# Kernel optimization log

Hardware: AMD Instinct MI355X
Metric: run time of the kernel (lower is better)

Reference implementation:

```python
import jax, jax.numpy as jnp
import numpy as np

N_EMBED = 1024
N_HEAD = 16
EPS = 1.1920929e-07  # torch.finfo(float32).eps, nn.RMSNorm default eps=None


def rmsnorm(x, w):
    var = jnp.mean(x * x, axis=-1, keepdims=True)
    return x * jax.lax.rsqrt(var + EPS) * w


def setup_inputs() -> dict:
    key = jax.random.key(0)
    ks = jax.random.split(key, 12)
    d = N_EMBED
    s = lambda fan_in: 1.0 / np.sqrt(fan_in)
    inp = {
        "x": jax.random.normal(ks[0], (2, 2048, d), jnp.float32),
        "w_attn": jax.random.uniform(ks[1], (d, 3 * d), jnp.float32, -s(d), s(d)),
        "b_attn": jax.random.uniform(ks[2], (3 * d,), jnp.float32, -s(d), s(d)),
        "w_proj": jax.random.uniform(ks[3], (d, d), jnp.float32, -s(d), s(d)),
        "b_proj": jax.random.uniform(ks[4], (d,), jnp.float32, -s(d), s(d)),
        "w_fc1": jax.random.uniform(ks[5], (d, 4 * d), jnp.float32, -s(d), s(d)),
        "b_fc1": jax.random.uniform(ks[6], (4 * d,), jnp.float32, -s(d), s(d)),
        "w_fc2": jax.random.uniform(ks[7], (4 * d, d), jnp.float32, -s(4 * d), s(4 * d)),
        "b_fc2": jax.random.uniform(ks[8], (d,), jnp.float32, -s(4 * d), s(4 * d)),
        "g_norm1": jnp.ones((d,), jnp.float32),
        "g_norm2": jnp.ones((d,), jnp.float32),
    }
    return inp


def reference(x, w_attn, b_attn, w_proj, b_proj, w_fc1, b_fc1, w_fc2, b_fc2, g_norm1, g_norm2):
    B, T, d = x.shape
    H = N_HEAD
    hd = d // H

    # --- attention branch ---
    h = rmsnorm(x, g_norm1)
    qkv = h @ w_attn + b_attn  # [B,T,3d]
    q, k, v = jnp.split(qkv, 3, axis=-1)
    q = q.reshape(B, T, H, hd).transpose(0, 2, 1, 3)  # [B,H,T,hd]
    k = k.reshape(B, T, H, hd).transpose(0, 2, 1, 3)
    v = v.reshape(B, T, H, hd).transpose(0, 2, 1, 3)
    qk = jnp.einsum('bhqd,bhkd->bhqk', q, k)  # NOTE: no logit scaling (as in source)
    mask = jnp.tril(jnp.ones((T, T), bool))
    qk = jnp.where(mask, qk, -jnp.inf)
    # source scales softmax OUTPUT by n_embed**-0.5 (faithful quirk)
    attn = jax.nn.softmax(qk, axis=-1) * (d ** -0.5)
    o = jnp.einsum('bhqk,bhkd->bhqd', attn, v)
    o = o.transpose(0, 2, 1, 3).reshape(B, T, d)
    x = x + (o @ w_proj + b_proj)

    # --- MLP branch ---
    h = rmsnorm(x, g_norm2)
    h = jax.nn.gelu(h @ w_fc1 + b_fc1, approximate=False)
    x = x + (h @ w_fc2 + b_fc2)
    return x
```

## Files before the change

### kernel.cpp

```cpp
#include <hip/hip_runtime.h>
#include <hip/hip_bf16.h>


typedef __hip_bfloat16 bf16;
typedef __attribute__((ext_vector_type(8))) short short8;
typedef __attribute__((ext_vector_type(4))) float floatx4;

__device__ __forceinline__ float bits2f(unsigned short u) {
  union { unsigned int i; float f; } c; c.i = ((unsigned int)u) << 16; return c.f;
}
__device__ __forceinline__ unsigned short f2bits(float f) {
  bf16 b = __float2bfloat16(f);
  union { bf16 b; unsigned short u; } c; c.b = b; return c.u;
}

__device__ __forceinline__ void gld_lds16(const unsigned short* g, unsigned short* l) {
  __builtin_amdgcn_global_load_lds(
      (const __attribute__((address_space(1))) void*)g,
      (__attribute__((address_space(3))) void*)l, 16, 0, 0);
}

__global__ __launch_bounds__(256) void rmsnorm_r18(const float* __restrict__ x,
                                                   const float* __restrict__ g,
                                                   unsigned short* __restrict__ out)
{
  const int row = blockIdx.x, tid = threadIdx.x;
  const size_t rb = (size_t)row * 1024;
  float4 xv = *(const float4*)(x + rb + tid * 4);
  float v[4] = {xv.x, xv.y, xv.z, xv.w};
  float s = v[0]*v[0] + v[1]*v[1] + v[2]*v[2] + v[3]*v[3];
  #pragma unroll
  for (int off = 32; off > 0; off >>= 1) s += __shfl_down(s, off, 64);
  __shared__ float part[4];
  if ((tid & 63) == 0) part[tid >> 6] = s;
  __syncthreads();
  const float tot = part[0] + part[1] + part[2] + part[3];
  const float sc = rsqrtf(tot * (1.0f / 1024.0f) + 1.1920929e-07f);
  float4 gv = *(const float4*)(g + tid * 4);
  ushort4 o4 = { f2bits(v[0] * sc * gv.x), f2bits(v[1] * sc * gv.y),
                 f2bits(v[2] * sc * gv.z), f2bits(v[3] * sc * gv.w) };
  *(ushort4*)(out + rb + tid * 4) = o4;
}

__global__ __launch_bounds__(256) void wprep_r18(const float* __restrict__ in,
                                                 unsigned short* __restrict__ out,
                                                 int K, int N)
{
  __shared__ unsigned short tile[32][33];
  const int tid = threadIdx.x;
  const int k0 = blockIdx.y * 32, n0 = blockIdx.x * 32;
  const int tr = tid >> 3, tc4 = (tid & 7) * 4;
  float4 v = *(const float4*)(in + (size_t)(k0 + tr) * N + n0 + tc4);
  tile[tr][tc4 + 0] = f2bits(v.x);
  tile[tr][tc4 + 1] = f2bits(v.y);
  tile[tr][tc4 + 2] = f2bits(v.z);
  tile[tr][tc4 + 3] = f2bits(v.w);
  __syncthreads();
  ushort4 o = { tile[tc4 + 0][tr], tile[tc4 + 1][tr],
                tile[tc4 + 2][tr], tile[tc4 + 3][tr] };
  *(ushort4*)(out + (size_t)(n0 + tr) * K + k0 + tc4) = o;
}

template<int EPI>
__global__ __launch_bounds__(256) void gemm128_r18(
    const unsigned short* __restrict__ A,
    const unsigned short* __restrict__ BT,
    const float* __restrict__ bias,
    const float* __restrict__ resid,
    void* __restrict__ Cout,
    int M, int N, int K, int Klen)
{
  __shared__ __align__(16) unsigned short As[2][128 * 32];
  __shared__ __align__(16) unsigned short Bs[2][128 * 32];
  const int tid = threadIdx.x;
  const int lane = tid & 63;
  const int wv = tid >> 6;
  const int m0 = blockIdx.y * 128, n0 = blockIdx.x * 128;
  const int wm = (wv >> 1) * 64, wn = (wv & 1) * 64;
  const int kbase = blockIdx.z * Klen;

  const int s0 = tid, s1 = tid + 256;
  const int r0 = s0 >> 2, kq0 = (s0 & 3) ^ ((r0 >> 1) & 3);
  const int r1 = s1 >> 2, kq1 = (s1 & 3) ^ ((r1 >> 1) & 3);
  const unsigned short* Ab = A  + (size_t)m0 * K;
  const unsigned short* Bb = BT + (size_t)n0 * K;
  const size_t ga0 = (size_t)r0 * K + kq0 * 8 + kbase;
  const size_t ga1 = (size_t)r1 * K + kq1 * 8 + kbase;

  floatx4 acc[4][4];
  #pragma unroll
  for (int i = 0; i < 4; ++i)
    #pragma unroll
    for (int j = 0; j < 4; ++j)
      acc[i][j] = (floatx4){0.f, 0.f, 0.f, 0.f};

  int aoff[4], boff[4];
  #pragma unroll
  for (int i = 0; i < 4; ++i) {
    int ra = wm + i * 16 + (lane & 15);
    aoff[i] = (ra * 4 + ((lane >> 4) ^ ((ra >> 1) & 3))) * 8;
    int rb = wn + i * 16 + (lane & 15);
    boff[i] = (rb * 4 + ((lane >> 4) ^ ((rb >> 1) & 3))) * 8;
  }

  gld_lds16(Ab + ga0, As[0] + s0 * 8);
  gld_lds16(Ab + ga1, As[0] + s1 * 8);
  gld_lds16(Bb + ga0, Bs[0] + s0 * 8);
  gld_lds16(Bb + ga1, Bs[0] + s1 * 8);
  __syncthreads();

  const int nsteps = Klen >> 5;
  for (int t = 0; t < nsteps; ++t) {
    const int cur = t & 1;
    if (t + 1 < nsteps) {
      const size_t ko = (size_t)(t + 1) * 32;
      gld_lds16(Ab + ga0 + ko, As[cur ^ 1] + s0 * 8);
      gld_lds16(Ab + ga1 + ko, As[cur ^ 1] + s1 * 8);
      gld_lds16(Bb + ga0 + ko, Bs[cur ^ 1] + s0 * 8);
      gld_lds16(Bb + ga1 + ko, Bs[cur ^ 1] + s1 * 8);
    }

    short8 af[4], bfr[4];
    #pragma unroll
    for (int i = 0; i < 4; ++i) {
      af[i]  = *(const short8*)(As[cur] + aoff[i]);
      bfr[i] = *(const short8*)(Bs[cur] + boff[i]);
    }
    #pragma unroll
    for (int i = 0; i < 4; ++i)
      #pragma unroll
      for (int j = 0; j < 4; ++j)
        acc[i][j] = __builtin_amdgcn_mfma_f32_16x16x32_bf16(af[i], bfr[j], acc[i][j], 0, 0, 0);

    __syncthreads();
  }

  float* Cp32 = (float*)Cout;
  if constexpr (EPI == 4) Cp32 += (size_t)blockIdx.z * ((size_t)M * N);

  #pragma unroll
  for (int i = 0; i < 4; ++i) {
    #pragma unroll
    for (int j = 0; j < 4; ++j) {
      const int rbase = m0 + wm + i * 16 + (lane >> 4) * 4;
      const int c = n0 + wn + j * 16 + (lane & 15);
      float bia = 0.0f;
      if constexpr (EPI != 4) bia = bias[c];
      #pragma unroll
      for (int r = 0; r < 4; ++r) {
        float v = acc[i][j][r] + bia;
        const size_t idx = (size_t)(rbase + r) * N + c;
        if constexpr (EPI == 0) {
          ((unsigned short*)Cout)[idx] = f2bits(v);
        } else if constexpr (EPI == 1) {
          ((float*)Cout)[idx] = v + resid[idx];
        } else if constexpr (EPI == 2) {
          v = 0.5f * v * (1.0f + erff(v * 0.70710678118654752f));
          ((unsigned short*)Cout)[idx] = f2bits(v);
        } else if constexpr (EPI == 3) {
          ((float*)Cout)[idx] = v + resid[idx];
        } else {
          Cp32[idx] = v;
        }
      }
    }
  }
}

template<int EPI>
__global__ __launch_bounds__(512) void gemm256_r18(
    const unsigned short* __restrict__ A,
    const unsigned short* __restrict__ BT,
    const float* __restrict__ bias,
    void* __restrict__ Cout,
    int M, int N, int K)
{
  __shared__ __align__(16) unsigned short As[4][256 * 32];
  __shared__ __align__(16) unsigned short Bs[4][256 * 32];
  const int tid = threadIdx.x;
  const int lane = tid & 63, wv = tid >> 6;
  const int quad = lane >> 4, l15 = lane & 15;
  const int m0 = blockIdx.y * 256, n0 = blockIdx.x * 256;
  const int wm = (wv >> 2) * 128, wn = (wv & 3) * 64;

  const int s0 = tid, s1 = tid + 512;
  const int r0 = s0 >> 2, kq0 = (s0 & 3) ^ ((r0 >> 1) & 3);
  const int r1 = s1 >> 2, kq1 = (s1 & 3) ^ ((r1 >> 1) & 3);
  const unsigned short* Ab = A  + (size_t)m0 * K;
  const unsigned short* Bb = BT + (size_t)n0 * K;
  const size_t ga0 = (size_t)r0 * K + kq0 * 8;
  const size_t ga1 = (size_t)r1 * K + kq1 * 8;

  floatx4 acc[8][4];
  #pragma unroll
  for (int i = 0; i < 8; ++i)
    #pragma unroll
    for (int j = 0; j < 4; ++j)
      acc[i][j] = (floatx4){0.f, 0.f, 0.f, 0.f};

  int aoff[8], boff[4];
  #pragma unroll
  for (int i = 0; i < 8; ++i) {
    int ra = wm + i * 16 + l15;
    aoff[i] = (ra * 4 + (quad ^ ((ra >> 1) & 3))) * 8;
  }
  #pragma unroll
  for (int j = 0; j < 4; ++j) {
    int rb = wn + j * 16 + l15;
    boff[j] = (rb * 4 + (quad ^ ((rb >> 1) & 3))) * 8;
  }

  #define STG_R18(t) { const size_t ko = (size_t)(t) * 32; const int bb = (t) & 3; \
    gld_lds16(Ab + ga0 + ko, As[bb] + s0 * 8); \
    gld_lds16(Ab + ga1 + ko, As[bb] + s1 * 8); \
    gld_lds16(Bb + ga0 + ko, Bs[bb] + s0 * 8); \
    gld_lds16(Bb + ga1 + ko, Bs[bb] + s1 * 8); }

  STG_R18(0);
  STG_R18(1);

  const int nsteps = K >> 5;
  for (int t = 0; t < nsteps; ++t) {
    const int cur = t & 3;
    if (t + 2 < nsteps) {
      STG_R18(t + 2);
      asm volatile("s_waitcnt vmcnt(8)" ::: "memory");
    } else if (t + 1 < nsteps) {
      asm volatile("s_waitcnt vmcnt(4)" ::: "memory");
    } else {
      asm volatile("s_waitcnt vmcnt(0)" ::: "memory");
    }
    __builtin_amdgcn_s_barrier();
    asm volatile("" ::: "memory");

    short8 bfr[4];
    #pragma unroll
    for (int j = 0; j < 4; ++j)
      bfr[j] = *(const short8*)(Bs[cur] + boff[j]);
    #pragma unroll
    for (int ih = 0; ih < 2; ++ih) {
      short8 af[4];
      #pragma unroll
      for (int k = 0; k < 4; ++k)
        af[k] = *(const short8*)(As[cur] + aoff[ih * 4 + k]);
      #pragma unroll
      for (int k = 0; k < 4; ++k)
        #pragma unroll
        for (int j = 0; j < 4; ++j)
          acc[ih * 4 + k][j] = __builtin_amdgcn_mfma_f32_16x16x32_bf16(af[k], bfr[j], acc[ih * 4 + k][j], 0, 0, 0);
    }
  }
  #undef STG_R18

  #pragma unroll
  for (int i = 0; i < 8; ++i) {
    #pragma unroll
    for (int j = 0; j < 4; ++j) {
      const int rbase = m0 + wm + i * 16 + quad * 4;
      const int c = n0 + wn + j * 16 + l15;
      const float bia = bias[c];
      #pragma unroll
      for (int r = 0; r < 4; ++r) {
        float v = acc[i][j][r] + bia;
        const size_t idx = (size_t)(rbase + r) * N + c;
        if constexpr (EPI == 2) {
          v = 0.5f * v * (1.0f + erff(v * 0.70710678118654752f));
        }
        ((unsigned short*)Cout)[idx] = f2bits(v);
      }
    }
  }
}

__global__ __launch_bounds__(256) void red2_r18(const float* __restrict__ P,
                                                const float* __restrict__ resid,
                                                const float* __restrict__ bias,
                                                float* __restrict__ out)
{
  const size_t i = ((size_t)blockIdx.x * 256 + threadIdx.x) * 4;
  const int col = (int)(i & 1023);
  float4 p0 = *(const float4*)(P + i);
  float4 p1 = *(const float4*)(P + ((size_t)4096 * 1024) + i);
  float4 xr = *(const float4*)(resid + i);
  float4 b  = *(const float4*)(bias + col);
  float4 o  = { p0.x + p1.x + xr.x + b.x, p0.y + p1.y + xr.y + b.y,
                p0.z + p1.z + xr.z + b.z, p0.w + p1.w + xr.w + b.w };
  *(float4*)(out + i) = o;
}

__global__ __launch_bounds__(512) void attn_r18(const unsigned short* __restrict__ qkv,
                                                unsigned short* __restrict__ o)
{
  __shared__ __align__(16) unsigned short Qs[128 * 64];
  __shared__ __align__(16) unsigned short Ks[2][128 * 64];
  __shared__ __align__(16) unsigned short VT[2][64 * 136];
  __shared__ __align__(16) unsigned short Ps[128 * 136];
  __shared__ __align__(16) float stat_s[128];

  const int tid = threadIdx.x, lane = tid & 63, wv = tid >> 6;
  const int quad = lane >> 4, l15 = lane & 15;
  const int qt0 = blockIdx.x, bh = blockIdx.y;
  const int b = bh >> 4, h = bh & 15;
  const size_t base = (size_t)b * 2048 * 3072;
  const int qcol = h * 64, kcol = 1024 + h * 64, vcol = 2048 + h * 64;

  const int sr = tid >> 3, scp = tid & 7, sc = scp ^ (sr & 7);
  const unsigned short* kgp = qkv + base + (size_t)sr * 3072 + kcol + sc * 8;
  const int vp = tid & 63, vdc = tid >> 6;
  const unsigned short* vgp = qkv + base + (size_t)(2 * vp) * 3072 + vcol + vdc * 8;

  for (int pass = 0; pass < 2; ++pass) {
    const int qt = pass ? qt0 : 15 - qt0;
    const int q0 = qt * 128;
    const int nkt = qt + 1;

    __syncthreads();

    #pragma unroll
    for (int p = 0; p < 2; ++p) {
      int s = tid + 512 * p;
      int r = s >> 3, cp = s & 7, c = cp ^ (r & 7);
      gld_lds16(qkv + base + (size_t)(q0 + r) * 3072 + qcol + c * 8, Qs + s * 8);
    }
    gld_lds16(kgp, Ks[0] + tid * 8);
    gld_lds16(kgp + (size_t)64 * 3072, Ks[0] + (size_t)(tid + 512) * 8);
    {
      uint4 u0 = *(const uint4*)vgp;
      uint4 u1 = *(const uint4*)(vgp + 3072);
      unsigned short* dst = VT[0] + (size_t)(vdc * 8) * 136 + 2 * vp;
      *(unsigned int*)(dst + 0 * 136) = (u0.x & 0xffffu) | (u1.x << 16);
      *(unsigned int*)(dst + 1 * 136) = (u0.x >> 16)     | (u1.x & 0xffff0000u);
      *(unsigned int*)(dst + 2 * 136) = (u0.y & 0xffffu) | (u1.y << 16);
      *(unsigned int*)(dst + 3 * 136) = (u0.y >> 16)     | (u1.y & 0xffff0000u);
      *(unsigned int*)(dst + 4 * 136) = (u0.z & 0xffffu) | (u1.z << 16);
      *(unsigned int*)(dst + 5 * 136) = (u0.z >> 16)     | (u1.z & 0xffff0000u);
      *(unsigned int*)(dst + 6 * 136) = (u0.w & 0xffffu) | (u1.w << 16);
      *(unsigned int*)(dst + 7 * 136) = (u0.w >> 16)     | (u1.w & 0xffff0000u);
    }
    __syncthreads();

    short8 qa[2];
    #pragma unroll
    for (int ks = 0; ks < 2; ++ks) {
      int ra = wv * 16 + l15;
      int cp = (ks * 4 + quad) ^ (ra & 7);
      qa[ks] = *(const short8*)(Qs + (ra * 8 + cp) * 8);
    }

    floatx4 oacc[4];
    #pragma unroll
    for (int dt = 0; dt < 4; ++dt) oacc[dt] = (floatx4){0.f, 0.f, 0.f, 0.f};
    float m_i[4], l_i[4];
    #pragma unroll
    for (int r = 0; r < 4; ++r) { m_i[r] = -3.0e38f; l_i[r] = 0.0f; }

    for (int kt = 0; kt < nkt; ++kt) {
      const int cur = kt & 1;
      const bool pf = (kt + 1 < nkt);
      uint4 u0, u1;
      if (pf) {
        const size_t koff = (size_t)(kt + 1) * 128 * 3072;
        gld_lds16(kgp + koff, Ks[cur ^ 1] + tid * 8);
        gld_lds16(kgp + koff + (size_t)64 * 3072, Ks[cur ^ 1] + (size_t)(tid + 512) * 8);
        u0 = *(const uint4*)(vgp + koff);
        u1 = *(const uint4*)(vgp + koff + 3072);
      }

      floatx4 s_[8];
      #pragma unroll
      for (int j = 0; j < 8; ++j) s_[j] = (floatx4){0.f, 0.f, 0.f, 0.f};
      #pragma unroll
      for (int j = 0; j < 8; ++j) {
        const int rb = j * 16 + l15;
        short8 kb0 = *(const short8*)(Ks[cur] + (rb * 8 + ((quad    ) ^ (rb & 7))) * 8);
        short8 kb1 = *(const short8*)(Ks[cur] + (rb * 8 + ((quad + 4) ^ (rb & 7))) * 8);
        s_[j] = __builtin_amdgcn_mfma_f32_16x16x32_bf16(qa[0], kb0, s_[j], 0, 0, 0);
        s_[j] = __builtin_amdgcn_mfma_f32_16x16x32_bf16(qa[1], kb1, s_[j], 0, 0, 0);
      }

      const int k0 = kt * 128;
      const int rowmin = q0 + wv * 16;
      const int rowb = rowmin + quad * 4;
      if (k0 + 127 > rowmin) {
        #pragma unroll
        for (int j = 0; j < 8; ++j) {
          const int col = k0 + j * 16 + l15;
          #pragma unroll
          for (int r = 0; r < 4; ++r)
            if (col > rowb + r) s_[j][r] = -3.0e38f;
        }
      }
      float fm[4], al[4], rs[4];
      #pragma unroll
      for (int r = 0; r < 4; ++r) {
        float a = fmaxf(fmaxf(s_[0][r], s_[1][r]), fmaxf(s_[2][r], s_[3][r]));
        float c = fmaxf(fmaxf(s_[4][r], s_[5][r]), fmaxf(s_[6][r], s_[7][r]));
        fm[r] = fmaxf(a, c);
      }
      #pragma unroll
      for (int msk = 1; msk < 16; msk <<= 1)
        #pragma unroll
        for (int r = 0; r < 4; ++r)
          fm[r] = fmaxf(fm[r], __shfl_xor(fm[r], msk, 64));
      #pragma unroll
      for (int r = 0; r < 4; ++r) {
        const float mn = fmaxf(m_i[r], fm[r]);
        al[r] = __expf(m_i[r] - mn);
        m_i[r] = mn;
      }
      #pragma unroll
      for (int j = 0; j < 8; ++j)
        #pragma unroll
        for (int r = 0; r < 4; ++r)
          s_[j][r] = __expf(s_[j][r] - m_i[r]);
      #pragma unroll
      for (int r = 0; r < 4; ++r) {
        float a = (s_[0][r] + s_[1][r]) + (s_[2][r] + s_[3][r]);
        float c = (s_[4][r] + s_[5][r]) + (s_[6][r] + s_[7][r]);
        rs[r] = a + c;
      }
      #pragma unroll
      for (int msk = 1; msk < 16; msk <<= 1)
        #pragma unroll
        for (int r = 0; r < 4; ++r)
          rs[r] += __shfl_xor(rs[r], msk, 64);
      #pragma unroll
      for (int r = 0; r < 4; ++r)
        l_i[r] = l_i[r] * al[r] + rs[r];
      if (l15 == 0) {
        float4 a4 = { al[0], al[1], al[2], al[3] };
        *(float4*)(stat_s + wv * 16 + quad * 4) = a4;
      }
      #pragma unroll
      for (int j = 0; j < 8; ++j)
        #pragma unroll
        for (int r = 0; r < 4; ++r)
          Ps[(size_t)(wv * 16 + quad * 4 + r) * 136 + j * 16 + l15] = f2bits(s_[j][r]);

      const float alq = stat_s[wv * 16 + l15];
      #pragma unroll
      for (int dt = 0; dt < 4; ++dt)
        #pragma unroll
        for (int r = 0; r < 4; ++r)
          oacc[dt][r] *= alq;

      short8 pb[4];
      #pragma unroll
      for (int ks = 0; ks < 4; ++ks)
        pb[ks] = *(const short8*)(Ps + (size_t)(wv * 16 + l15) * 136 + ks * 32 + quad * 8);
      #pragma unroll
      for (int dt = 0; dt < 4; ++dt) {
        short8 va[4];
        #pragma unroll
        for (int ks = 0; ks < 4; ++ks)
          va[ks] = *(const short8*)(VT[cur] + (size_t)(dt * 16 + l15) * 136 + ks * 32 + quad * 8);
        #pragma unroll
        for (int ks = 0; ks < 4; ++ks)
          oacc[dt] = __builtin_amdgcn_mfma_f32_16x16x32_bf16(va[ks], pb[ks], oacc[dt], 0, 0, 0);
      }

      if (pf) {
        unsigned short* dst = VT[cur ^ 1] + (size_t)(vdc * 8) * 136 + 2 * vp;
        *(unsigned int*)(dst + 0 * 136) = (u0.x & 0xffffu) | (u1.x << 16);
        *(unsigned int*)(dst + 1 * 136) = (u0.x >> 16)     | (u1.x & 0xffff0000u);
        *(unsigned int*)(dst + 2 * 136) = (u0.y & 0xffffu) | (u1.y << 16);
        *(unsigned int*)(dst + 3 * 136) = (u0.y >> 16)     | (u1.y & 0xffff0000u);
        *(unsigned int*)(dst + 4 * 136) = (u0.z & 0xffffu) | (u1.z << 16);
        *(unsigned int*)(dst + 5 * 136) = (u0.z >> 16)     | (u1.z & 0xffff0000u);
        *(unsigned int*)(dst + 6 * 136) = (u0.w & 0xffffu) | (u1.w << 16);
        *(unsigned int*)(dst + 7 * 136) = (u0.w >> 16)     | (u1.w & 0xffff0000u);
      }
      __syncthreads();
    }

    if (l15 == 0) {
      float4 l4 = { l_i[0], l_i[1], l_i[2], l_i[3] };
      *(float4*)(stat_s + wv * 16 + quad * 4) = l4;
    }
    const float linv = 0.03125f / stat_s[wv * 16 + l15];
    const size_t row = (size_t)b * 2048 + q0 + wv * 16 + l15;
    #pragma unroll
    for (int dt = 0; dt < 4; ++dt) {
      const int col = h * 64 + dt * 16 + quad * 4;
      ushort4 o4 = { f2bits(oacc[dt][0] * linv), f2bits(oacc[dt][1] * linv),
                     f2bits(oacc[dt][2] * linv), f2bits(oacc[dt][3] * linv) };
      *(ushort4*)(o + row * 1024 + col) = o4;
    }
  }
}

extern "C" void kernel_launch(void* const* d_in, const int* in_sizes, int n_in,
                              void* d_out, int out_size, void* d_ws, size_t ws_size,
                              hipStream_t stream)
{
  (void)in_sizes; (void)n_in; (void)out_size; (void)ws_size;
  const float* x      = (const float*)d_in[0];
  const float* w_attn = (const float*)d_in[1];
  const float* b_attn = (const float*)d_in[2];
  const float* w_proj = (const float*)d_in[3];
  const float* b_proj = (const float*)d_in[4];
  const float* w_fc1  = (const float*)d_in[5];
  const float* b_fc1  = (const float*)d_in[6];
  const float* w_fc2  = (const float*)d_in[7];
  const float* b_fc2  = (const float*)d_in[8];
  const float* g1     = (const float*)d_in[9];
  const float* g2     = (const float*)d_in[10];
  float* out = (float*)d_out;

  char* ws = (char*)d_ws;
  unsigned short* h   = (unsigned short*)(ws);
  unsigned short* qkv = (unsigned short*)(ws + ((size_t)8  << 20));
  unsigned short* ov  = (unsigned short*)(ws);
  float*          x1  = (float*)         (ws + ((size_t)32 << 20));
  unsigned short* h2  = (unsigned short*)(ws + ((size_t)8  << 20));
  unsigned short* h3  = (unsigned short*)(ws + ((size_t)48 << 20));
  unsigned short* WT  = (unsigned short*)(ws + ((size_t)80 << 20));
  float*          P   = (float*)(ws);

  const int M = 4096;

  rmsnorm_r18<<<M, 256, 0, stream>>>(x, g1, h);
  wprep_r18<<<dim3(3072 / 32, 1024 / 32), 256, 0, stream>>>(w_attn, WT, 1024, 3072);
  gemm256_r18<0><<<dim3(3072 / 256, M / 256), 512, 0, stream>>>(h, WT, b_attn, qkv, M, 3072, 1024);
  attn_r18<<<dim3(8, 32), 512, 0, stream>>>(qkv, ov);
  wprep_r18<<<dim3(1024 / 32, 1024 / 32), 256, 0, stream>>>(w_proj, WT, 1024, 1024);
  gemm128_r18<1><<<dim3(1024 / 128, M / 128), 256, 0, stream>>>(ov, WT, b_proj, x, x1, M, 1024, 1024, 1024);
  rmsnorm_r18<<<M, 256, 0, stream>>>(x1, g2, h2);
  wprep_r18<<<dim3(4096 / 32, 1024 / 32), 256, 0, stream>>>(w_fc1, WT, 1024, 4096);
  gemm256_r18<2><<<dim3(4096 / 256, M / 256), 512, 0, stream>>>(h2, WT, b_fc1, h3, M, 4096, 1024);
  wprep_r18<<<dim3(1024 / 32, 4096 / 32), 256, 0, stream>>>(w_fc2, WT, 4096, 1024);
  gemm128_r18<4><<<dim3(1024 / 128, M / 128, 2), 256, 0, stream>>>(h3, WT, nullptr, nullptr, P, M, 1024, 4096, 2048);
  red2_r18<<<4096, 256, 0, stream>>>(P, x1, b_fc2, out);
}
```

Measured before the change: 370.0 us.

## Add XCD-aware block swizzle, MFMA setprio, and split A-fragment loads in GEMMs

Adds an XCD swizzle that remaps block indices so consecutive tiles land on the same XCD, aiming for better L2 reuse in both GEMM kernels. Wraps MFMA sequences in s_setprio(1)/s_setprio(0) in the GEMM and attention kernels so waves issuing matrix ops get scheduling priority. In the 128 GEMM it also splits the A-fragment loads into two halves interleaved with MFMAs to overlap LDS reads with compute. The swizzle also applies to the split-K launch; it only remaps x/y and covers the full grid, so correctness holds.

Measured after the change: 362.7 us. Within noise of the previous version (-2.0%).

```diff
diff --git a/kernel.cpp b/kernel.cpp
--- a/kernel.cpp
+++ b/kernel.cpp
@@ -20,7 +20,17 @@
       (__attribute__((address_space(3))) void*)l, 16, 0, 0);
 }
 
-__global__ __launch_bounds__(256) void rmsnorm_r18(const float* __restrict__ x,
+__device__ __forceinline__ void xcd_swz(int& bx, int& by) {
+  const int gx = gridDim.x, nwg = gx * gridDim.y;
+  int bid = by * gx + bx;
+  const int q = nwg >> 3, r = nwg & 7;
+  const int x = bid & 7, yq = bid >> 3;
+  int sb = (x < r) ? (x * (q + 1) + yq) : (r * (q + 1) + (x - r) * q + yq);
+  bx = sb % gx;
+  by = sb / gx;
+}
+
+__global__ __launch_bounds__(256) void rmsnorm_r19(const float* __restrict__ x,
                                                    const float* __restrict__ g,
                                                    unsigned short* __restrict__ out)
 {
@@ -42,7 +52,7 @@
   *(ushort4*)(out + rb + tid * 4) = o4;
 }
 
-__global__ __launch_bounds__(256) void wprep_r18(const float* __restrict__ in,
+__global__ __launch_bounds__(256) void wprep_r19(const float* __restrict__ in,
                                                  unsigned short* __restrict__ out,
                                                  int K, int N)
 {
@@ -62,7 +72,7 @@
 }
 
 template<int EPI>
-__global__ __launch_bounds__(256) void gemm128_r18(
+__global__ __launch_bounds__(256) void gemm128_r19(
     const unsigned short* __restrict__ A,
     const unsigned short* __restrict__ BT,
     const float* __restrict__ bias,
@@ -75,7 +85,9 @@
   const int tid = threadIdx.x;
   const int lane = tid & 63;
   const int wv = tid >> 6;
-  const int m0 = blockIdx.y * 128, n0 = blockIdx.x * 128;
+  int bxs = blockIdx.x, bys = blockIdx.y;
+  xcd_swz(bxs, bys);
+  const int m0 = bys * 128, n0 = bxs * 128;
   const int wm = (wv >> 1) * 64, wn = (wv & 1) * 64;
   const int kbase = blockIdx.z * Klen;
 
@@ -120,17 +132,31 @@
       gld_lds16(Bb + ga1 + ko, Bs[cur ^ 1] + s1 * 8);
     }
 
-    short8 af[4], bfr[4];
-    #pragma unroll
-    for (int i = 0; i < 4; ++i) {
-      af[i]  = *(const short8*)(As[cur] + aoff[i]);
-      bfr[i] = *(const short8*)(Bs[cur] + boff[i]);
-    }
-    #pragma unroll
-    for (int i = 0; i < 4; ++i)
+    short8 bfr[4], af01[2];
+    #pragma unroll
+    for (int j = 0; j < 4; ++j)
+      bfr[j] = *(const short8*)(Bs[cur] + boff[j]);
+    #pragma unroll
+    for (int i = 0; i < 2; ++i)
+      af01[i] = *(const short8*)(As[cur] + aoff[i]);
+    __builtin_amdgcn_s_setprio(1);
+    #pragma unroll
+    for (int i = 0; i < 2; ++i)
       #pragma unroll
       for (int j = 0; j < 4; ++j)
-        acc[i][j] = __builtin_amdgcn_mfma_f32_16x16x32_bf16(af[i], bfr[j], acc[i][j], 0, 0, 0);
+        acc[i][j] = __builtin_amdgcn_mfma_f32_16x16x32_bf16(af01[i], bfr[j], acc[i][j], 0, 0, 0);
+    __builtin_amdgcn_s_setprio(0);
+    short8 af23[2];
+    #pragma unroll
+    for (int i = 0; i < 2; ++i)
+      af23[i] = *(const short8*)(As[cur] + aoff[2 + i]);
+    __builtin_amdgcn_s_setprio(1);
+    #pragma unroll
+    for (int i = 0; i < 2; ++i)
+      #pragma unroll
+      for (int j = 0; j < 4; ++j)
+        acc[2 + i][j] = __builtin_amdgcn_mfma_f32_16x16x32_bf16(af23[i], bfr[j], acc[2 + i][j], 0, 0, 0);
+    __builtin_amdgcn_s_setprio(0);
 
     __syncthreads();
   }
@@ -168,7 +194,7 @@
 }
 
 template<int EPI>
-__global__ __launch_bounds__(512) void gemm256_r18(
+__global__ __launch_bounds__(512) void gemm256_r19(
     const unsigned short* __restrict__ A,
     const unsigned short* __restrict__ BT,
     const float* __restrict__ bias,
@@ -180,7 +206,9 @@
   const int tid = threadIdx.x;
   const int lane = tid & 63, wv = tid >> 6;
   const int quad = lane >> 4, l15 = lane & 15;
-  const int m0 = blockIdx.y * 256, n0 = blockIdx.x * 256;
+  int bxs = blockIdx.x, bys = blockIdx.y;
+  xcd_swz(bxs, bys);
+  const int m0 = bys * 256, n0 = bxs * 256;
   const int wm = (wv >> 2) * 128, wn = (wv & 3) * 64;
 
   const int s0 = tid, s1 = tid + 512;
@@ -210,20 +238,20 @@
     boff[j] = (rb * 4 + (quad ^ ((rb >> 1) & 3))) * 8;
   }
 
-  #define STG_R18(t) { const size_t ko = (size_t)(t) * 32; const int bb = (t) & 3; \
+  #define STG_R19(t) { const size_t ko = (size_t)(t) * 32; const int bb = (t) & 3; \
     gld_lds16(Ab + ga0 + ko, As[bb] + s0 * 8); \
     gld_lds16(Ab + ga1 + ko, As[bb] + s1 * 8); \
     gld_lds16(Bb + ga0 + ko, Bs[bb] + s0 * 8); \
     gld_lds16(Bb + ga1 + ko, Bs[bb] + s1 * 8); }
 
-  STG_R18(0);
-  STG_R18(1);
+  STG_R19(0);
+  STG_R19(1);
 
   const int nsteps = K >> 5;
   for (int t = 0; t < nsteps; ++t) {
     const int cur = t & 3;
     if (t + 2 < nsteps) {
-      STG_R18(t + 2);
+      STG_R19(t + 2);
       asm volatile("s_waitcnt vmcnt(8)" ::: "memory");
     } else if (t + 1 < nsteps) {
       asm volatile("s_waitcnt vmcnt(4)" ::: "memory");
@@ -243,14 +271,16 @@
       #pragma unroll
       for (int k = 0; k < 4; ++k)
         af[k] = *(const short8*)(As[cur] + aoff[ih * 4 + k]);
+      __builtin_amdgcn_s_setprio(1);
       #pragma unroll
       for (int k = 0; k < 4; ++k)
         #pragma unroll
         for (int j = 0; j < 4; ++j)
           acc[ih * 4 + k][j] = __builtin_amdgcn_mfma_f32_16x16x32_bf16(af[k], bfr[j], acc[ih * 4 + k][j], 0, 0, 0);
-    }
-  }
-  #undef STG_R18
+      __builtin_amdgcn_s_setprio(0);
+    }
+  }
+  #undef STG_R19
 
   #pragma unroll
   for (int i = 0; i < 8; ++i) {
@@ -272,7 +302,7 @@
   }
 }
 
-__global__ __launch_bounds__(256) void red2_r18(const float* __restrict__ P,
+__global__ __launch_bounds__(256) void red2_r19(const float* __restrict__ P,
                                                 const float* __restrict__ resid,
                                                 const float* __restrict__ bias,
                                                 float* __restrict__ out)
@@ -288,7 +318,7 @@
   *(float4*)(out + i) = o;
 }
 
-__global__ __launch_bounds__(512) void attn_r18(const unsigned short* __restrict__ qkv,
+__global__ __launch_bounds__(512) void attn_r19(const unsigned short* __restrict__ qkv,
                                                 unsigned short* __restrict__ o)
 {
   __shared__ __align__(16) unsigned short Qs[128 * 64];
@@ -369,6 +399,7 @@
       floatx4 s_[8];
       #pragma unroll
       for (int j = 0; j < 8; ++j) s_[j] = (floatx4){0.f, 0.f, 0.f, 0.f};
+      __builtin_amdgcn_s_setprio(1);
       #pragma unroll
       for (int j = 0; j < 8; ++j) {
         const int rb = j * 16 + l15;
@@ -377,6 +408,7 @@
         s_[j] = __builtin_amdgcn_mfma_f32_16x16x32_bf16(qa[0], kb0, s_[j], 0, 0, 0);
         s_[j] = __builtin_amdgcn_mfma_f32_16x16x32_bf16(qa[1], kb1, s_[j], 0, 0, 0);
       }
+      __builtin_amdgcn_s_setprio(0);
 
       const int k0 = kt * 128;
       const int rowmin = q0 + wv * 16;
@@ -448,6 +480,7 @@
       #pragma unroll
       for (int ks = 0; ks < 4; ++ks)
         pb[ks] = *(const short8*)(Ps + (size_t)(wv * 16 + l15) * 136 + ks * 32 + quad * 8);
+      __builtin_amdgcn_s_setprio(1);
       #pragma unroll
       for (int dt = 0; dt < 4; ++dt) {
         short8 va[4];
@@ -458,6 +491,7 @@
         for (int ks = 0; ks < 4; ++ks)
           oacc[dt] = __builtin_amdgcn_mfma_f32_16x16x32_bf16(va[ks], pb[ks], oacc[dt], 0, 0, 0);
       }
+      __builtin_amdgcn_s_setprio(0);
 
       if (pf) {
         unsigned short* dst = VT[cur ^ 1] + (size_t)(vdc * 8) * 136 + 2 * vp;
@@ -519,16 +553,16 @@
 
   const int M = 4096;
 
-  rmsnorm_r18<<<M, 256, 0, stream>>>(x, g1, h);
-  wprep_r18<<<dim3(3072 / 32, 1024 / 32), 256, 0, stream>>>(w_attn, WT, 1024, 3072);
-  gemm256_r18<0><<<dim3(3072 / 256, M / 256), 512, 0, stream>>>(h, WT, b_attn, qkv, M, 3072, 1024);
-  attn_r18<<<dim3(8, 32), 512, 0, stream>>>(qkv, ov);
-  wprep_r18<<<dim3(1024 / 32, 1024 / 32), 256, 0, stream>>>(w_proj, WT, 1024, 1024);
-  gemm128_r18<1><<<dim3(1024 / 128, M / 128), 256, 0, stream>>>(ov, WT, b_proj, x, x1, M, 1024, 1024, 1024);
-  rmsnorm_r18<<<M, 256, 0, stream>>>(x1, g2, h2);
-  wprep_r18<<<dim3(4096 / 32, 1024 / 32), 256, 0, stream>>>(w_fc1, WT, 1024, 4096);
-  gemm256_r18<2><<<dim3(4096 / 256, M / 256), 512, 0, stream>>>(h2, WT, b_fc1, h3, M, 4096, 1024);
-  wprep_r18<<<dim3(1024 / 32, 4096 / 32), 256, 0, stream>>>(w_fc2, WT, 4096, 1024);
-  gemm128_r18<4><<<dim3(1024 / 128, M / 128, 2), 256, 0, stream>>>(h3, WT, nullptr, nullptr, P, M, 1024, 4096, 2048);
-  red2_r18<<<4096, 256, 0, stream>>>(P, x1, b_fc2, out);
-}
+  rmsnorm_r19<<<M, 256, 0, stream>>>(x, g1, h);
+  wprep_r19<<<dim3(3072 / 32, 1024 / 32), 256, 0, stream>>>(w_attn, WT, 1024, 3072);
+  gemm256_r19<0><<<dim3(3072 / 256, M / 256), 512, 0, stream>>>(h, WT, b_attn, qkv, M, 3072, 1024);
+  attn_r19<<<dim3(8, 32), 512, 0, stream>>>(qkv, ov);
+  wprep_r19<<<dim3(1024 / 32, 1024 / 32), 256, 0, stream>>>(w_proj, WT, 1024, 1024);
+  gemm128_r19<1><<<dim3(1024 / 128, M / 128), 256, 0, stream>>>(ov, WT, b_proj, x, x1, M, 1024, 1024, 1024);
+  rmsnorm_r19<<<M, 256, 0, stream>>>(x1, g2, h2);
+  wprep_r19<<<dim3(4096 / 32, 1024 / 32), 256, 0, stream>>>(w_fc1, WT, 1024, 4096);
+  gemm256_r19<2><<<dim3(4096 / 256, M / 256), 512, 0, stream>>>(h2, WT, b_fc1, h3, M, 4096, 1024);
+  wprep_r19<<<dim3(1024 / 32, 4096 / 32), 256, 0, stream>>>(w_fc2, WT, 4096, 1024);
+  gemm128_r19<4><<<dim3(1024 / 128, M / 128, 2), 256, 0, stream>>>(h3, WT, nullptr, nullptr, P, M, 1024, 4096, 2048);
+  red2_r19<<<4096, 256, 0, stream>>>(P, x1, b_fc2, out);
+}
```
